# Kernel tuning notes

Measured on AMD Instinct MI355X. Metric: run time of the kernel, lower is better.

The kernel has to match this reference:

```python
import jax, jax.numpy as jnp
import numpy as np

B, IMG, TXT, DIM, H, D = 1, 1024, 256, 1536, 24, 64
SCALE = 1.0  # control cross-attn scale


def _lin(x, w, b):
    return x @ w + b


def _heads(x):  # [B,S,DIM] -> [B,H,S,D]
    return jnp.swapaxes(x.reshape(x.shape[0], x.shape[1], H, D), 1, 2)


def _merge(x):  # [B,H,S,D] -> [B,S,DIM]
    return jnp.swapaxes(x, 1, 2).reshape(x.shape[0], x.shape[2], H * D)


def _sdpa(q, k, v):
    s = jnp.einsum('bhqd,bhkd->bhqk', q, k) * (1.0 / np.sqrt(D))
    return jnp.einsum('bhqk,bhkd->bhqd', jax.nn.softmax(s, axis=-1), v)


def _rope(x, pe):  # x: [B,H,S,D], pe: [1,1,S,D//2,2,2]
    xr = x.reshape(*x.shape[:-1], -1, 1, 2)  # [B,H,S,D/2,1,2]
    out = pe[..., 0] * xr[..., 0] + pe[..., 1] * xr[..., 1]  # [B,H,S,D/2,2]
    return out.reshape(x.shape)


def _forward(hidden_states, encoder_hidden_states, hidden_states_control,
             encoder_hidden_states_control, img_to_q_control, pe,
             a_q_w, a_q_b, a_k_w, a_k_b, a_v_w, a_v_b,
             a_addq_w, a_addq_b, a_addk_w, a_addk_b, a_addv_w, a_addv_b,
             a_out_w, a_out_b, a_addout_w, a_addout_b,
             c_q_w, c_q_b, c_k_w, c_k_b, c_v_w, c_v_b,
             c_addq_w, c_addq_b, c_addk_w, c_addk_b, c_addv_w, c_addv_b,
             c_out_w, c_out_b, c_addout_w, c_addout_b):
    img_len = hidden_states.shape[1]
    # ---- main joint attention stream (no RoPE, per original) ----
    q = jnp.concatenate([_heads(_lin(hidden_states, a_q_w, a_q_b)),
                         _heads(_lin(encoder_hidden_states, a_addq_w, a_addq_b))], axis=2)
    k = jnp.concatenate([_heads(_lin(hidden_states, a_k_w, a_k_b)),
                         _heads(_lin(encoder_hidden_states, a_addk_w, a_addk_b))], axis=2)
    v = jnp.concatenate([_heads(_lin(hidden_states, a_v_w, a_v_b)),
                         _heads(_lin(encoder_hidden_states, a_addv_w, a_addv_b))], axis=2)
    hs = _merge(_sdpa(q, k, v))
    hs, ehs = hs[:, :img_len], hs[:, img_len:]
    # ---- control joint attention stream (with RoPE) ----
    qc = jnp.concatenate([_heads(_lin(hidden_states_control, c_q_w, c_q_b)),
                          _heads(_lin(encoder_hidden_states_control, c_addq_w, c_addq_b))], axis=2)
    kc = jnp.concatenate([_heads(_lin(hidden_states_control, c_k_w, c_k_b)),
                          _heads(_lin(encoder_hidden_states_control, c_addk_w, c_addk_b))], axis=2)
    vc = jnp.concatenate([_heads(_lin(hidden_states_control, c_v_w, c_v_b)),
                          _heads(_lin(encoder_hidden_states_control, c_addv_w, c_addv_b))], axis=2)
    key_cross, value_cross = kc, vc  # saved BEFORE RoPE, per original
    hsc = _merge(_sdpa(_rope(qc, pe), _rope(kc, pe), vc))
    hsc, ehsc = hsc[:, :img_len], hsc[:, img_len:]
    # ---- cross attention: img query attends to control K/V ----
    q_cross = _rope(_heads(img_to_q_control), pe[:, :, :img_len])
    k_cross = _rope(key_cross, pe[:, :, :key_cross.shape[2]])
    cross = _merge(_sdpa(q_cross, k_cross, value_cross))
    hs = hs + SCALE * cross
    # ---- output projections (to_out[1] is dropout p=0 -> identity) ----
    hs = _lin(hs, a_out_w, a_out_b)
    ehs = _lin(ehs, a_addout_w, a_addout_b)
    hsc = _lin(hsc, c_out_w, c_out_b)
    ehsc = _lin(ehsc, c_addout_w, c_addout_b)
    return hs, ehs, hsc, ehsc


def setup_inputs() -> dict:
    key = jax.random.key(0)
    ki = iter(jax.random.split(key, 80))
    d = {}
    d['hidden_states'] = jax.random.normal(next(ki), (B, IMG, DIM), jnp.float32)
    d['encoder_hidden_states'] = jax.random.normal(next(ki), (B, TXT, DIM), jnp.float32)
    d['hidden_states_control'] = jax.random.normal(next(ki), (B, IMG, DIM), jnp.float32)
    d['encoder_hidden_states_control'] = jax.random.normal(next(ki), (B, TXT, DIM), jnp.float32)
    d['img_to_q_control'] = jax.random.normal(next(ki), (B, IMG, DIM), jnp.float32)
    # realistic rotary pe: [1,1,S,D/2,2,2] rotation matrices
    S = IMG + TXT
    pos = np.arange(S, dtype=np.float32)
    freqs = 1.0 / (10000.0 ** (np.arange(0, D, 2, dtype=np.float32) / D))  # [D/2]
    ang = pos[:, None] * freqs[None, :]  # [S, D/2]
    cos, sin = np.cos(ang), np.sin(ang)
    pe = np.stack([np.stack([cos, -sin], -1), np.stack([sin, cos], -1)], -2)  # [S,D/2,2,2]
    d['pe'] = jnp.asarray(pe)[None, None]
    for p in ('a', 'c'):
        for name in ('q', 'k', 'v', 'addq', 'addk', 'addv', 'out', 'addout'):
            d[f'{p}_{name}_w'] = jax.random.normal(next(ki), (DIM, DIM), jnp.float32) * 0.02
            d[f'{p}_{name}_b'] = jax.random.normal(next(ki), (DIM,), jnp.float32) * 0.01
    return d


def reference(hidden_states, encoder_hidden_states, hidden_states_control,
              encoder_hidden_states_control, img_to_q_control, pe,
              a_q_w, a_q_b, a_k_w, a_k_b, a_v_w, a_v_b,
              a_addq_w, a_addq_b, a_addk_w, a_addk_b, a_addv_w, a_addv_b,
              a_out_w, a_out_b, a_addout_w, a_addout_b,
              c_q_w, c_q_b, c_k_w, c_k_b, c_v_w, c_v_b,
              c_addq_w, c_addq_b, c_addk_w, c_addk_b, c_addv_w, c_addv_b,
              c_out_w, c_out_b, c_addout_w, c_addout_b):
    return _forward(hidden_states, encoder_hidden_states, hidden_states_control,
                    encoder_hidden_states_control, img_to_q_control, pe,
                    a_q_w, a_q_b, a_k_w, a_k_b, a_v_w, a_v_b,
                    a_addq_w, a_addq_b, a_addk_w, a_addk_b, a_addv_w, a_addv_b,
                    a_out_w, a_out_b, a_addout_w, a_addout_b,
                    c_q_w, c_q_b, c_k_w, c_k_b, c_v_w, c_v_b,
                    c_addq_w, c_addq_b, c_addk_w, c_addk_b, c_addv_w, c_addv_b,
                    c_out_w, c_out_b, c_addout_w, c_addout_b)
```

## Files before the change

### kernel.cpp

```cpp
#include <hip/hip_runtime.h>

#define DIM 1536
#define IMG 1024
#define TXT 256
#define SEQ 1280
#define NH 24
#define HD 64
#define SD ((size_t)SEQ * DIM)
#define IDSZ ((size_t)IMG * DIM)
#define WSZ ((size_t)DIM * DIM)

typedef __attribute__((ext_vector_type(8))) short short8;
typedef __attribute__((ext_vector_type(4))) float f32x4;

__device__ __forceinline__ float bf2f(ushort u) {
    union { unsigned int i; float f; } v; v.i = ((unsigned int)u) << 16; return v.f;
}
__device__ __forceinline__ ushort f2bf(float f) {
    union { unsigned int i; float f; } v; v.f = f;
    unsigned int u = v.i;
    u += 0x7fffu + ((u >> 16) & 1u);
    return (ushort)(u >> 16);
}

__global__ __launch_bounds__(256) void detect_dtype(const void* __restrict__ p,
                                                    int* __restrict__ flag)
{
    __shared__ int cnt;
    if (threadIdx.x == 0) cnt = 0;
    __syncthreads();
    const ushort* u = (const ushort*)p;
    int local = 0;
    for (int i = threadIdx.x; i < 2048; i += 256) {
        ushort v = u[2 * i];
        int e = (v >> 7) & 0xFF;
        if (e >= 0xC0) local++;
    }
    atomicAdd(&cnt, local);
    __syncthreads();
    if (threadIdx.x == 0) flag[0] = (cnt > 16) ? 1 : 0;
}

struct CvtP {
    const void* src[16];
    ushort* dst[16];
    int n8[16];
};

__global__ __launch_bounds__(256) void convert_bf16(CvtP p, const int* __restrict__ dflag)
{
    const int a = blockIdx.y;
    const int i = blockIdx.x * 256 + threadIdx.x;
    if (i >= p.n8[a]) return;
    const size_t off = (size_t)i * 8;
    uint4 o;
    if (dflag[0]) {
        const float* s = (const float*)p.src[a] + off;
        const float4 f0 = *(const float4*)s;
        const float4 f1 = *(const float4*)(s + 4);
        ushort t[8];
        t[0] = f2bf(f0.x); t[1] = f2bf(f0.y); t[2] = f2bf(f0.z); t[3] = f2bf(f0.w);
        t[4] = f2bf(f1.x); t[5] = f2bf(f1.y); t[6] = f2bf(f1.z); t[7] = f2bf(f1.w);
        o = *(uint4*)t;
    } else {
        o = *(const uint4*)((const ushort*)p.src[a] + off);
    }
    *(uint4*)(p.dst[a] + off) = o;
}

#define LSTR 40

struct QKV3P {
    const ushort* Xb;
    const ushort* Wb;
    const void* B[12];
    float* Y[6];
    ushort* Yh[6];
    ushort* Yl[6];
};

__global__ __launch_bounds__(256) void gemm_qkv_v4(QKV3P p, const int* __restrict__ dflag)
{
    __shared__ __align__(16) ushort As[2][128 * LSTR];
    __shared__ __align__(16) ushort Bs[2][64 * 64];
    const int dt = dflag[0];
    const int bx = blockIdx.x;
    const int wsel = bx / 12;
    const int n0 = (bx - wsel * 12) * 128;
    const int ys = blockIdx.y;
    const int str = (ys >= 10) ? 1 : 0;
    const int m0g = (ys - str * 10) * 128;
    const bool istxt = (m0g >= IMG);
    const int widx = str * 6 + wsel + (istxt ? 3 : 0);
    const ushort* X  = p.Xb + (size_t)str * SD;
    const ushort* Wp = p.Wb + (size_t)widx * WSZ;
    const void* Bp = p.B[widx];
    const int yidx = str * 3 + wsel;
    float*  Y  = p.Y[yidx];
    ushort* yh = p.Yh[yidx];
// ... 50 lines not shown
    loadA(0); loadB(0);
    storeA(0); storeB(0);
    __syncthreads();

    for (int k = 0; k < DIM / 32; ++k) {
        const int cur = k & 1;
        const bool hn = (k + 1) < DIM / 32;
        if (hn) { loadA((k + 1) * 32); loadB((k + 1) * 32); }

        short8 b[4];
#pragma unroll
        for (int j = 0; j < 4; ++j) {
            const int rrn = wn + j * 16 + l16;
            const int R = rrn & 63, half = rrn >> 6;
            const int gx = (((half << 2) + quad) ^ (R & 7) ^ (R >> 3)) & 7;
            b[j] = *(const short8*)&Bs[cur][R * 64 + gx * 8];
        }
#pragma unroll
        for (int i = 0; i < 4; ++i) {
            const int rr = wm + i * 16 + l16;
            const int ps = (quad >> 1) ^ ((rr >> 3) & 1);
            const int col = ps * 16 + (quad & 1) * 8;
            short8 a = *(const short8*)&As[cur][rr * LSTR + col];
#pragma unroll
            for (int j = 0; j < 4; ++j)
                acc[i][j] = __builtin_amdgcn_mfma_f32_16x16x32_bf16(a, b[j], acc[i][j], 0, 0, 0);
        }
        if (hn) { storeA(cur ^ 1); storeB(cur ^ 1); }
        __syncthreads();
    }

#pragma unroll
    for (int j = 0; j < 4; ++j) {
        const int col = n0 + wn + j * 16 + l16;
        const float bv = dt ? ((const float*)Bp)[col] : bf2f(((const ushort*)Bp)[col]);
#pragma unroll
        for (int i = 0; i < 4; ++i)
#pragma unroll
            for (int r = 0; r < 4; ++r) {
                const int row = m0g + wm + i * 16 + quad * 4 + r;
                const size_t o = (size_t)row * DIM + col;
                const float val = acc[i][j][r] + bv;
                if (Y) Y[o] = val;
                if (yh) {
                    const ushort hv = f2bf(val);
                    yh[o] = hv;
                    yl[o] = f2bf(val - bf2f(hv));
                }
            }
    }
}

struct OutP {
    const float* X;
    const void* W[4]; const void* B[4];
    void* out;
};

__global__ __launch_bounds__(256) void gemm_out_v3(OutP p, const int* __restrict__ dflag)
{
    __shared__ __align__(16) ushort Ah[2][64 * LSTR];
    __shared__ __align__(16) ushort Al[2][64 * LSTR];
    __shared__ __align__(16) ushort Bs[2][64 * 64];
    const int dt = dflag[0];
    const int n0 = blockIdx.x * 128;
    const int mt = blockIdx.y;
    const int seg = (mt < 16) ? 0 : (mt < 20) ? 1 : (mt < 36) ? 2 : 3;
    const void* Wp = p.W[seg];
    const void* Bp = p.B[seg];
    const int m0 = mt * 64;

    const int t = threadIdx.x;
    const int wave = t >> 6, lane = t & 63;
    const int quad = lane >> 4, l16 = lane & 15;
    const int wm = (wave >> 1) * 32, wn = (wave & 1) * 64;

    const int arow = t >> 2, ag = t & 3;
    const int apg = ag >> 1, asub = ag & 1;
    const int aps = apg ^ ((arow >> 3) & 1);
    const int adst = arow * LSTR + aps * 16 + asub * 8;
    const int bn8 = (t & 15) << 3, bkk = (t >> 4) << 1;
    const int bkg = bkk >> 3, bo = bkk & 7;

    f32x4 acc[2][4];
#pragma unroll
    for (int i = 0; i < 2; ++i)
#pragma unroll
        for (int j = 0; j < 4; ++j) acc[i][j] = (f32x4)(0.0f);

    float4 raf[2];
    float4 rbf[4]; uint4 rbu[2];

    auto loadA = [&](int k0) {
        const float* xp = p.X + (size_t)(m0 + arow) * DIM + k0 + ag * 8;
        raf[0] = *(const float4*)xp;
        raf[1] = *(const float4*)(xp + 4);
    };
    auto loadB = [&](int k0) {
        const size_t off = (size_t)(k0 + bkk) * DIM + n0 + bn8;
        if (dt) {
            const float* wp0 = (const float*)Wp + off;
            rbf[0] = *(const float4*)wp0;         rbf[1] = *(const float4*)(wp0 + 4);
            rbf[2] = *(const float4*)(wp0 + DIM); rbf[3] = *(const float4*)(wp0 + DIM + 4);
        } else {
            const ushort* wp0 = (const ushort*)Wp + off;
            rbu[0] = *(const uint4*)wp0;
            rbu[1] = *(const uint4*)(wp0 + DIM);
        }
    };
    auto storeA = [&](int buf) {
        ushort hi[8], lo[8];
        const float* xs = (const float*)raf;
#pragma unroll
        for (int i = 0; i < 8; ++i) {
            hi[i] = f2bf(xs[i]);
            lo[i] = f2bf(xs[i] - bf2f(hi[i]));
        }
        *(uint4*)&Ah[buf][adst] = *(uint4*)&hi[0];
        *(uint4*)&Al[buf][adst] = *(uint4*)&lo[0];
    };
    auto storeB = [&](int buf) {
        ushort t0[8], t1[8];
        if (dt) {
            const float* f = (const float*)rbf;
#pragma unroll
            for (int j = 0; j < 8; ++j) { t0[j] = f2bf(f[j]); t1[j] = f2bf(f[8 + j]); }
        } else {
            *(uint4*)t0 = rbu[0];
            *(uint4*)t1 = rbu[1];
        }
#pragma unroll
        for (int j = 0; j < 8; ++j) {
            const int rr = bn8 + j;
            const int R = rr & 63, half = rr >> 6;
            const int gx = (((half << 2) + bkg) ^ (R & 7) ^ (R >> 3)) & 7;
            *(unsigned int*)&Bs[buf][R * 64 + gx * 8 + bo] =
                (unsigned int)t0[j] | ((unsigned int)t1[j] << 16);
        }
    };

    loadA(0); loadB(0);
    storeA(0); storeB(0);
    __syncthreads();

    for (int k = 0; k < DIM / 32; ++k) {
        const int cur = k & 1;
        const bool hn = (k + 1) < DIM / 32;
        if (hn) { loadA((k + 1) * 32); loadB((k + 1) * 32); }

        short8 b[4];
#pragma unroll
        for (int j = 0; j < 4; ++j) {
            const int rrn = wn + j * 16 + l16;
            const int R = rrn & 63, half = rrn >> 6;
            const int gx = (((half << 2) + quad) ^ (R & 7) ^ (R >> 3)) & 7;
            b[j] = *(const short8*)&Bs[cur][R * 64 + gx * 8];
        }
#pragma unroll
        for (int i = 0; i < 2; ++i) {
            const int rr = wm + i * 16 + l16;
            const int ps = (quad >> 1) ^ ((rr >> 3) & 1);
            const int col = ps * 16 + (quad & 1) * 8;
            short8 ah = *(const short8*)&Ah[cur][rr * LSTR + col];
            short8 al = *(const short8*)&Al[cur][rr * LSTR + col];
#pragma unroll
            for (int j = 0; j < 4; ++j) {
                acc[i][j] = __builtin_amdgcn_mfma_f32_16x16x32_bf16(ah, b[j], acc[i][j], 0, 0, 0);
                acc[i][j] = __builtin_amdgcn_mfma_f32_16x16x32_bf16(al, b[j], acc[i][j], 0, 0, 0);
            }
        }
        if (hn) { storeA(cur ^ 1); storeB(cur ^ 1); }
        __syncthreads();
    }

#pragma unroll
    for (int j = 0; j < 4; ++j) {
        const int col = n0 + wn + j * 16 + l16;
        const float bv = dt ? ((const float*)Bp)[col] : bf2f(((const ushort*)Bp)[col]);
#pragma unroll
        for (int i = 0; i < 2; ++i)
#pragma unroll
            for (int r = 0; r < 4; ++r) {
                const int grow = m0 + wm + i * 16 + quad * 4 + r;
                const size_t o = (size_t)grow * DIM + col;
                const float val = acc[i][j][r] + bv;
                if (dt) ((float*)p.out)[o] = val;
                else    ((ushort*)p.out)[o] = f2bf(val);
            }
    }
}

__device__ __forceinline__ void pe_load(const void* pe, int dt, size_t off,
                                        float& c00, float& c01, float& c10, float& c11)
{
    if (dt) {
        float4 pv = *(const float4*)((const float*)pe + off);
        c00 = pv.x; c01 = pv.y; c10 = pv.z; c11 = pv.w;
    } else {
        const ushort* pp = (const ushort*)pe + off;
        c00 = bf2f(pp[0]); c01 = bf2f(pp[1]); c10 = bf2f(pp[2]); c11 = bf2f(pp[3]);
    }
}

__global__ __launch_bounds__(256) void rope_f32_inplace(
    float* __restrict__ buf, const void* __restrict__ pe,
    const int* __restrict__ dflag, int S)
{
    const int dt = dflag[0];
    int idx = blockIdx.x * 256 + threadIdx.x;
    if (idx >= S * 768) return;
    int s = idx / 768, pp = idx - s * 768;
    int col = pp << 1, i = pp & 31;
    float* bp = buf + (size_t)s * DIM + col;
    float x0 = bp[0], x1 = bp[1];
    float c00, c01, c10, c11;
    pe_load(pe, dt, (size_t)s * 128 + i * 4, c00, c01, c10, c11);
    bp[0] = c00 * x0 + c01 * x1;
    bp[1] = c10 * x0 + c11 * x1;
}

__global__ __launch_bounds__(256) void rope_f32_to_split(
    const float* __restrict__ src, const void* __restrict__ pe,
    ushort* __restrict__ dh, ushort* __restrict__ dl,
    const int* __restrict__ dflag, int S)
{
    const int dt = dflag[0];
    int idx = blockIdx.x * 256 + threadIdx.x;
    if (idx >= S * 768) return;
    int s = idx / 768, pp = idx - s * 768;
    int col = pp << 1, i = pp & 31;
    float2 xv = *(const float2*)(src + (size_t)s * DIM + col);
    float c00, c01, c10, c11;
    pe_load(pe, dt, (size_t)s * 128 + i * 4, c00, c01, c10, c11);
    float y0 = c00 * xv.x + c01 * xv.y;
    float y1 = c10 * xv.x + c11 * xv.y;
    ushort h0 = f2bf(y0), h1 = f2bf(y1);
    ushort l0 = f2bf(y0 - bf2f(h0)), l1 = f2bf(y1 - bf2f(h1));
    *(unsigned int*)(dh + (size_t)s * DIM + col) = (unsigned int)h0 | ((unsigned int)h1 << 16);
    *(unsigned int*)(dl + (size_t)s * DIM + col) = (unsigned int)l0 | ((unsigned int)l1 << 16);
}

__global__ __launch_bounds__(256) void rope_in_to_f32(
    const void* __restrict__ src, const void* __restrict__ pe,
    float* __restrict__ dst, const int* __restrict__ dflag, int S)
{
    const int dt = dflag[0];
    int idx = blockIdx.x * 256 + threadIdx.x;
    if (idx >= S * 768) return;
    int s = idx / 768, pp = idx - s * 768;
    int col = pp << 1, i = pp & 31;
    float x0, x1;
    if (dt) {
        float2 xv = *(const float2*)((const float*)src + (size_t)s * DIM + col);
        x0 = xv.x; x1 = xv.y;
    } else {
        const ushort* sp = (const ushort*)src + (size_t)s * DIM + col;
        x0 = bf2f(sp[0]); x1 = bf2f(sp[1]);
    }
    float c00, c01, c10, c11;
    pe_load(pe, dt, (size_t)s * 128 + i * 4, c00, c01, c10, c11);
    float* dp = dst + (size_t)s * DIM + col;
    dp[0] = c00 * x0 + c01 * x1;
    dp[1] = c10 * x0 + c11 * x1;
}

__global__ __launch_bounds__(256) void vtrans_split(
    const float* __restrict__ V, ushort* __restrict__ Vth, ushort* __restrict__ Vtl,
    int seq)
{
    __shared__ unsigned int tile[64 * 65];
    const int s0 = blockIdx.x * 64;
    const int h = blockIdx.y;
    const int t = threadIdx.x;
#pragma unroll
    for (int it = 0; it < 16; ++it) {
        const int sl = (t >> 6) + (it << 2);
        const int d = t & 63;
        const float v = V[(size_t)(s0 + sl) * DIM + h * HD + d];
        const ushort hv = f2bf(v);
        const ushort lv = f2bf(v - bf2f(hv));
        tile[d * 65 + sl] = (unsigned int)hv | ((unsigned int)lv << 16);
    }
    __syncthreads();
    const int d = t >> 2, cc = (t & 3) << 4;
    ushort th[16], tl[16];
#pragma unroll
    for (int j = 0; j < 16; ++j) {
        const unsigned int w = tile[d * 65 + cc + j];
        th[j] = (ushort)w;
        tl[j] = (ushort)(w >> 16);
    }
    const size_t off = (size_t)(h * HD + d) * seq + s0 + cc;
    *(uint4*)(Vth + off)     = *(uint4*)&th[0];
    *(uint4*)(Vth + off + 8) = *(uint4*)&th[8];
    *(uint4*)(Vtl + off)     = *(uint4*)&tl[0];
    *(uint4*)(Vtl + off + 8) = *(uint4*)&tl[8];
}

__device__ __forceinline__ int swz(int row, int col) {
    return row * 64 + ((((col >> 3) ^ row) & 7) << 3) + (col & 7);
}
__device__ __forceinline__ short8 ldfrag(const ushort* plane, int row, int col) {
    return *(const short8*)&plane[swz(row, col)];
}

struct AttnP {
    const float* Qf;
    const ushort *Kh, *Kl, *Vth, *Vtl;
    float* Op0;
    float* Op1;
    float2* Ml;
    int kvchunk;
    int kvstride;
};

__global__ __launch_bounds__(256) void attn_mfma_split(AttnP p)
{
    __shared__ ushort Qh_[4096], Ql_[4096];
    __shared__ ushort Kh_[4096], Kl_[4096];
    __shared__ ushort Vh_[4096], Vl_[4096];

    const int q0 = blockIdx.x * 64;
    const int h = blockIdx.y;
    const int z = blockIdx.z;
    const int t = threadIdx.x;
    const int wave = t >> 6, lane = t & 63;
    const int quad = lane >> 4, l16 = lane & 15;
    const int wq0 = wave * 16;

    const int srow = t >> 2, c0 = (t & 3) << 4;
    const int g0 = c0 >> 3;
    const int p0 = ((g0 ^ (srow & 7)) & 7) << 3;
    const int p1 = (((g0 + 1) ^ (srow & 7)) & 7) << 3;

    {
        const float* src = p.Qf + (size_t)(q0 + srow) * DIM + h * HD + c0;
        float x[16];
        *(float4*)&x[0]  = *(const float4*)(src);
        *(float4*)&x[4]  = *(const float4*)(src + 4);
        *(float4*)&x[8]  = *(const float4*)(src + 8);
        *(float4*)&x[12] = *(const float4*)(src + 12);
        ushort hi[16], lo[16];
#pragma unroll
        for (int i = 0; i < 16; ++i) {
            hi[i] = f2bf(x[i]);
            lo[i] = f2bf(x[i] - bf2f(hi[i]));
        }
        *(uint4*)&Qh_[srow * 64 + p0] = *(uint4*)&hi[0];
        *(uint4*)&Qh_[srow * 64 + p1] = *(uint4*)&hi[8];
        *(uint4*)&Ql_[srow * 64 + p0] = *(uint4*)&lo[0];
        *(uint4*)&Ql_[srow * 64 + p1] = *(uint4*)&lo[8];
    }
    short8 qfh[2], qfl[2];
#pragma unroll
    for (int c = 0; c < 2; ++c) {
        qfh[c] = ldfrag(Qh_, wq0 + l16, c * 32 + quad * 8);
        qfl[c] = ldfrag(Ql_, wq0 + l16, c * 32 + quad * 8);
    }

    float m_[4], l_[4];
#pragma unroll
    for (int r = 0; r < 4; ++r) { m_[r] = -3e38f; l_[r] = 0.0f; }
    f32x4 Oacc[4];
#pragma unroll
    for (int j = 0; j < 4; ++j) Oacc[j] = (f32x4)(0.0f);

    const int kvbeg = z * p.kvchunk;
    for (int kt = 0; kt < p.kvchunk; kt += 64) {
        const int kv0 = kvbeg + kt;
        __syncthreads();
        {
            const size_t off = (size_t)(kv0 + srow) * DIM + h * HD + c0;
            *(uint4*)&Kh_[srow * 64 + p0] = *(const uint4*)(p.Kh + off);
            *(uint4*)&Kh_[srow * 64 + p1] = *(const uint4*)(p.Kh + off + 8);
            *(uint4*)&Kl_[srow * 64 + p0] = *(const uint4*)(p.Kl + off);
            *(uint4*)&Kl_[srow * 64 + p1] = *(const uint4*)(p.Kl + off + 8);
        }
        {
            const size_t off = (size_t)(h * HD + srow) * p.kvstride + kv0 + c0;
            *(uint4*)&Vh_[srow * 64 + p0] = *(const uint4*)(p.Vth + off);
            *(uint4*)&Vh_[srow * 64 + p1] = *(const uint4*)(p.Vth + off + 8);
            *(uint4*)&Vl_[srow * 64 + p0] = *(const uint4*)(p.Vtl + off);
            *(uint4*)&Vl_[srow * 64 + p1] = *(const uint4*)(p.Vtl + off + 8);
        }
        __syncthreads();

        f32x4 S[4];
#pragma unroll
        for (int j = 0; j < 4; ++j) S[j] = (f32x4)(0.0f);
#pragma unroll
        for (int c = 0; c < 2; ++c) {
#pragma unroll
            for (int j = 0; j < 4; ++j) {
                short8 bh = ldfrag(Kh_, j * 16 + l16, c * 32 + quad * 8);
                short8 bl = ldfrag(Kl_, j * 16 + l16, c * 32 + quad * 8);
                S[j] = __builtin_amdgcn_mfma_f32_16x16x32_bf16(qfh[c], bh, S[j], 0, 0, 0);
                S[j] = __builtin_amdgcn_mfma_f32_16x16x32_bf16(qfl[c], bh, S[j], 0, 0, 0);
                S[j] = __builtin_amdgcn_mfma_f32_16x16x32_bf16(qfh[c], bl, S[j], 0, 0, 0);
            }
        }
#pragma unroll
        for (int j = 0; j < 4; ++j)
#pragma unroll
            for (int r = 0; r < 4; ++r) S[j][r] *= 0.125f;

        float alpha[4];
#pragma unroll
        for (int r = 0; r < 4; ++r) {
            float mx = fmaxf(fmaxf(S[0][r], S[1][r]), fmaxf(S[2][r], S[3][r]));
            mx = fmaxf(mx, __shfl_xor(mx, 1));
            mx = fmaxf(mx, __shfl_xor(mx, 2));
            mx = fmaxf(mx, __shfl_xor(mx, 4));
            mx = fmaxf(mx, __shfl_xor(mx, 8));
            float mn = fmaxf(m_[r], mx);
            alpha[r] = __expf(m_[r] - mn);
            m_[r] = mn;
            float rs = 0.0f;
#pragma unroll
            for (int j = 0; j < 4; ++j) {
                float pv = __expf(S[j][r] - mn);
                S[j][r] = pv;
                rs += pv;
            }
            rs += __shfl_xor(rs, 1);
            rs += __shfl_xor(rs, 2);
            rs += __shfl_xor(rs, 4);
            rs += __shfl_xor(rs, 8);
            l_[r] = l_[r] * alpha[r] + rs;
        }
#pragma unroll
        for (int j = 0; j < 4; ++j)
#pragma unroll
            for (int r = 0; r < 4; ++r) Oacc[j][r] *= alpha[r];

        {
            const int prow = wq0 + quad * 4;
#pragma unroll
            for (int j = 0; j < 4; ++j)
#pragma unroll
                for (int r = 0; r < 4; ++r) {
                    float pv = S[j][r];
                    ushort ph = f2bf(pv);
                    ushort pl = f2bf(pv - bf2f(ph));
                    int idx = swz(prow + r, j * 16 + l16);
                    Qh_[idx] = ph;
                    Ql_[idx] = pl;
                }
        }

#pragma unroll
        for (int c = 0; c < 2; ++c) {
            short8 pah = ldfrag(Qh_, wq0 + l16, c * 32 + quad * 8);
            short8 pal = ldfrag(Ql_, wq0 + l16, c * 32 + quad * 8);
#pragma unroll
            for (int jn = 0; jn < 4; ++jn) {
                short8 vbh = ldfrag(Vh_, jn * 16 + l16, c * 32 + quad * 8);
                short8 vbl = ldfrag(Vl_, jn * 16 + l16, c * 32 + quad * 8);
                Oacc[jn] = __builtin_amdgcn_mfma_f32_16x16x32_bf16(pah, vbh, Oacc[jn], 0, 0, 0);
                Oacc[jn] = __builtin_amdgcn_mfma_f32_16x16x32_bf16(pal, vbh, Oacc[jn], 0, 0, 0);
                Oacc[jn] = __builtin_amdgcn_mfma_f32_16x16x32_bf16(pah, vbl, Oacc[jn], 0, 0, 0);
            }
        }
    }

    float* Opz = z ? p.Op1 : p.Op0;
#pragma unroll
    for (int r = 0; r < 4; ++r) {
        const int rowq = q0 + wq0 + quad * 4 + r;
        if (l16 == 0)
            p.Ml[((size_t)z * NH + h) * SEQ + rowq] = make_float2(m_[r], l_[r]);
#pragma unroll
        for (int jn = 0; jn < 4; ++jn)
            Opz[(size_t)rowq * DIM + h * HD + jn * 16 + l16] = Oacc[jn][r];
    }
}

__global__ __launch_bounds__(256) void attn_merge(
    const float* __restrict__ Op0, const float* __restrict__ Op1,
    const float2* __restrict__ Ml,
    float* __restrict__ out, const float* __restrict__ addto, int qlen)
{
    const int idx = blockIdx.x * 256 + threadIdx.x;
    if (idx >= qlen * 384) return;
    const int rowq = idx / 384;
    const int c4 = (idx - rowq * 384) << 2;
    const float2 a = Ml[(size_t)(c4 >> 6) * SEQ + rowq];
    const float2 b = Ml[(size_t)(NH + (c4 >> 6)) * SEQ + rowq];
    const float ms = fmaxf(a.x, b.x);
    const float s0 = __expf(a.x - ms), s1 = __expf(b.x - ms);
    const float inv = 1.0f / (s0 * a.y + s1 * b.y);
    const float4 o0 = *(const float4*)&Op0[(size_t)rowq * DIM + c4];
    const float4 o1 = *(const float4*)&Op1[(size_t)rowq * DIM + c4];
    float4 r;
    r.x = (s0 * o0.x + s1 * o1.x) * inv;
    r.y = (s0 * o0.y + s1 * o1.y) * inv;
    r.z = (s0 * o0.z + s1 * o1.z) * inv;
    r.w = (s0 * o0.w + s1 * o1.w) * inv;
    if (addto) {
        const float4 c = *(const float4*)&addto[(size_t)rowq * DIM + c4];
        r.x += c.x; r.y += c.y; r.z += c.z; r.w += c.w;
    }
    *(float4*)&out[(size_t)rowq * DIM + c4] = r;
}

extern "C" void kernel_launch(void* const* d_in, const int* in_sizes, int n_in,
                              void* d_out, int out_size, void* d_ws, size_t ws_size,
                              hipStream_t stream) {
    (void)in_sizes; (void)n_in; (void)out_size; (void)ws_size;
    const void* hs   = d_in[0];
    const void* ehs  = d_in[1];
    const void* hsc  = d_in[2];
    const void* ehsc = d_in[3];
    const void* i2q  = d_in[4];
    const void* pe   = d_in[5];
#define W_(i) ((const void*)d_in[i])

    int*   flag = (int*)d_ws;
    float* fb = (float*)((char*)d_ws + 256);
    float* q1 = fb;
    float* k1 = q1 + SD;
    float* v1 = k1 + SD;
    float* vC = v1 + SD;
    float* oA = vC + SD;
    float* oC = oA + SD;
    ushort* kh  = (ushort*)(oC + SD);
    ushort* klo = kh + SD;
    ushort* vth = klo + SD;
    ushort* vtl = vth + SD;
    ushort* Wbf = vtl + SD;
    ushort* Xbf = Wbf + 12 * WSZ;
    float2* Ml = (float2*)(Xbf + 2 * SD);
    float* qA = oC;
    float* qx = k1;

    dim3 blk(256);
    detect_dtype<<<1, blk, 0, stream>>>(hs, flag);

    {
        CvtP cp;
        const int wsrc[12] = {6, 8, 10, 12, 14, 16, 22, 24, 26, 28, 30, 32};
        for (int j = 0; j < 12; ++j) {
            cp.src[j] = W_(wsrc[j]);
            cp.dst[j] = Wbf + (size_t)j * WSZ;
            cp.n8[j] = (int)(WSZ / 8);
        }
        cp.src[12] = hs;   cp.dst[12] = Xbf;                cp.n8[12] = (int)(IDSZ / 8);
        cp.src[13] = ehs;  cp.dst[13] = Xbf + IDSZ;         cp.n8[13] = (int)((size_t)TXT * DIM / 8);
        cp.src[14] = hsc;  cp.dst[14] = Xbf + SD;           cp.n8[14] = (int)(IDSZ / 8);
        cp.src[15] = ehsc; cp.dst[15] = Xbf + SD + IDSZ;    cp.n8[15] = (int)((size_t)TXT * DIM / 8);
        convert_bf16<<<dim3((int)(WSZ / 8 + 255) / 256, 16), blk, 0, stream>>>(cp, flag);
    }

    QKV3P qp;
    qp.Xb = Xbf;
    qp.Wb = Wbf;
    {
        const int bsrc[12] = {7, 9, 11, 13, 15, 17, 23, 25, 27, 29, 31, 33};
        for (int j = 0; j < 12; ++j) qp.B[j] = W_(bsrc[j]);
    }
    for (int j = 0; j < 6; ++j) { qp.Y[j] = nullptr; qp.Yh[j] = nullptr; qp.Yl[j] = nullptr; }
    qp.Y[0] = qA;
    qp.Yh[1] = kh;  qp.Yl[1] = klo;
    qp.Y[2] = v1;
    qp.Y[3] = q1;
    qp.Y[4] = k1;
    qp.Y[5] = vC;
    gemm_qkv_v4<<<dim3(36, 20), blk, 0, stream>>>(qp, flag);

    auto ATTN = [&](const float* Qfp, int qblocks, float* Op0, float* Op1) {
        AttnP p;
        p.Qf = Qfp;
        p.Kh = kh;  p.Kl = klo;
        p.Vth = vth; p.Vtl = vtl;
        p.Op0 = Op0; p.Op1 = Op1; p.Ml = Ml;
        p.kvchunk = SEQ / 2; p.kvstride = SEQ;
        attn_mfma_split<<<dim3(qblocks, NH, 2), blk, 0, stream>>>(p);
    };

    vtrans_split<<<dim3(SEQ / 64, NH), blk, 0, stream>>>(v1, vth, vtl, SEQ);
    ATTN(qA, SEQ / 64, v1, oA);
    attn_merge<<<(SEQ * 384 + 255) / 256, blk, 0, stream>>>(v1, oA, Ml, oA, nullptr, SEQ);

    rope_f32_inplace<<<(SEQ * 768 + 255) / 256, blk, 0, stream>>>(q1, pe, flag, SEQ);
    rope_f32_to_split<<<(SEQ * 768 + 255) / 256, blk, 0, stream>>>(k1, pe, kh, klo, flag, SEQ);
    vtrans_split<<<dim3(SEQ / 64, NH), blk, 0, stream>>>(vC, vth, vtl, SEQ);
    rope_in_to_f32<<<(IMG * 768 + 255) / 256, blk, 0, stream>>>(i2q, pe, qx, flag, IMG);

    ATTN(q1, SEQ / 64, v1, vC);
    attn_merge<<<(SEQ * 384 + 255) / 256, blk, 0, stream>>>(v1, vC, Ml, oC, nullptr, SEQ);

    ATTN(qx, IMG / 64, v1, vC);
    attn_merge<<<(IMG * 384 + 255) / 256, blk, 0, stream>>>(v1, vC, Ml, oA, oA, IMG);

    OutP op;
    op.X = oA;
    op.W[0] = W_(18); op.B[0] = W_(19);
    op.W[1] = W_(20); op.B[1] = W_(21);
    op.W[2] = W_(34); op.B[2] = W_(35);
    op.W[3] = W_(36); op.B[3] = W_(37);
    op.out = d_out;
    gemm_out_v3<<<dim3(12, 40), blk, 0, stream>>>(op, flag);
#undef W_
}
```

Measured before the change: 654.9 us.

## Batch all attention passes into one launch and fuse prep and merge kernels

Merges the three separate attention launches into a single attn_all grid that indexes per-segment Q/K/V pointers. Each stream now gets its own K/V buffers, so the passes no longer serialize through shared scratch. The vtrans and three RoPE kernels are folded into one prep_fused launch, and the three attn_merge launches become one merge_all that writes bf16 hi/lo split activations directly. The output projection weights are pre-converted to bf16 in the convert pass, so gemm_out no longer converts per tile. The change also adds s_setprio around the MFMA loops, at the cost of more workspace memory and an extra weight conversion.

```diff
diff --git a/kernel.cpp b/kernel.cpp
--- a/kernel.cpp
+++ b/kernel.cpp
@@ -42,9 +42,9 @@
 }
 
 struct CvtP {
-    const void* src[16];
-    ushort* dst[16];
-    int n8[16];
+    const void* src[20];
+    ushort* dst[20];
+    int n8[20];
 };
 
 __global__ __launch_bounds__(256) void convert_bf16(CvtP p, const int* __restrict__ dflag)
@@ -201,12 +201,13 @@
 }
 
 struct OutP {
-    const float* X;
-    const void* W[4]; const void* B[4];
+    const ushort* Xh; const ushort* Xl;
+    const ushort* Wb;
+    const void* B[4];
     void* out;
 };
 
-__global__ __launch_bounds__(256) void gemm_out_v3(OutP p, const int* __restrict__ dflag)
+__global__ __launch_bounds__(256) void gemm_out_v4(OutP p, const int* __restrict__ dflag)
 {
     __shared__ __align__(16) ushort Ah[2][64 * LSTR];
     __shared__ __align__(16) ushort Al[2][64 * LSTR];
@@ -215,7 +216,7 @@
     const int n0 = blockIdx.x * 128;
     const int mt = blockIdx.y;
     const int seg = (mt < 16) ? 0 : (mt < 20) ? 1 : (mt < 36) ? 2 : 3;
-    const void* Wp = p.W[seg];
+    const ushort* Wp = p.Wb + (size_t)seg * WSZ;
     const void* Bp = p.B[seg];
     const int m0 = mt * 64;
 
@@ -237,47 +238,27 @@
 #pragma unroll
         for (int j = 0; j < 4; ++j) acc[i][j] = (f32x4)(0.0f);
 
-    float4 raf[2];
-    float4 rbf[4]; uint4 rbu[2];
+    uint4 rah, ral;
+    uint4 rbu[2];
 
     auto loadA = [&](int k0) {
-        const float* xp = p.X + (size_t)(m0 + arow) * DIM + k0 + ag * 8;
-        raf[0] = *(const float4*)xp;
-        raf[1] = *(const float4*)(xp + 4);
+        const size_t off = (size_t)(m0 + arow) * DIM + k0 + ag * 8;
+        rah = *(const uint4*)(p.Xh + off);
+        ral = *(const uint4*)(p.Xl + off);
     };
     auto loadB = [&](int k0) {
-        const size_t off = (size_t)(k0 + bkk) * DIM + n0 + bn8;
-        if (dt) {
-            const float* wp0 = (const float*)Wp + off;
-            rbf[0] = *(const float4*)wp0;         rbf[1] = *(const float4*)(wp0 + 4);
-            rbf[2] = *(const float4*)(wp0 + DIM); rbf[3] = *(const float4*)(wp0 + DIM + 4);
-        } else {
-            const ushort* wp0 = (const ushort*)Wp + off;
-            rbu[0] = *(const uint4*)wp0;
-            rbu[1] = *(const uint4*)(wp0 + DIM);
-        }
+        const ushort* wp0 = Wp + (size_t)(k0 + bkk) * DIM + n0 + bn8;
+        rbu[0] = *(const uint4*)wp0;
+        rbu[1] = *(const uint4*)(wp0 + DIM);
     };
     auto storeA = [&](int buf) {
-        ushort hi[8], lo[8];
-        const float* xs = (const float*)raf;
-#pragma unroll
-        for (int i = 0; i < 8; ++i) {
-            hi[i] = f2bf(xs[i]);
-            lo[i] = f2bf(xs[i] - bf2f(hi[i]));
-        }
-        *(uint4*)&Ah[buf][adst] = *(uint4*)&hi[0];
-        *(uint4*)&Al[buf][adst] = *(uint4*)&lo[0];
+        *(uint4*)&Ah[buf][adst] = rah;
+        *(uint4*)&Al[buf][adst] = ral;
     };
     auto storeB = [&](int buf) {
         ushort t0[8], t1[8];
-        if (dt) {
-            const float* f = (const float*)rbf;
-#pragma unroll
-            for (int j = 0; j < 8; ++j) { t0[j] = f2bf(f[j]); t1[j] = f2bf(f[8 + j]); }
-        } else {
-            *(uint4*)t0 = rbu[0];
-            *(uint4*)t1 = rbu[1];
-        }
+        *(uint4*)t0 = rbu[0];
+        *(uint4*)t1 = rbu[1];
 #pragma unroll
         for (int j = 0; j < 8; ++j) {
             const int rr = bn8 + j;
@@ -351,99 +332,104 @@
     }
 }
 
-__global__ __launch_bounds__(256) void rope_f32_inplace(
-    float* __restrict__ buf, const void* __restrict__ pe,
-    const int* __restrict__ dflag, int S)
-{
-    const int dt = dflag[0];
-    int idx = blockIdx.x * 256 + threadIdx.x;
-    if (idx >= S * 768) return;
-    int s = idx / 768, pp = idx - s * 768;
-    int col = pp << 1, i = pp & 31;
-    float* bp = buf + (size_t)s * DIM + col;
-    float x0 = bp[0], x1 = bp[1];
-    float c00, c01, c10, c11;
-    pe_load(pe, dt, (size_t)s * 128 + i * 4, c00, c01, c10, c11);
-    bp[0] = c00 * x0 + c01 * x1;
-    bp[1] = c10 * x0 + c11 * x1;
-}
-
-__global__ __launch_bounds__(256) void rope_f32_to_split(
-    const float* __restrict__ src, const void* __restrict__ pe,
-    ushort* __restrict__ dh, ushort* __restrict__ dl,
-    const int* __restrict__ dflag, int S)
-{
-    const int dt = dflag[0];
-    int idx = blockIdx.x * 256 + threadIdx.x;
-    if (idx >= S * 768) return;
-    int s = idx / 768, pp = idx - s * 768;
-    int col = pp << 1, i = pp & 31;
-    float2 xv = *(const float2*)(src + (size_t)s * DIM + col);
-    float c00, c01, c10, c11;
-    pe_load(pe, dt, (size_t)s * 128 + i * 4, c00, c01, c10, c11);
-    float y0 = c00 * xv.x + c01 * xv.y;
-    float y1 = c10 * xv.x + c11 * xv.y;
-    ushort h0 = f2bf(y0), h1 = f2bf(y1);
-    ushort l0 = f2bf(y0 - bf2f(h0)), l1 = f2bf(y1 - bf2f(h1));
-    *(unsigned int*)(dh + (size_t)s * DIM + col) = (unsigned int)h0 | ((unsigned int)h1 << 16);
-    *(unsigned int*)(dl + (size_t)s * DIM + col) = (unsigned int)l0 | ((unsigned int)l1 << 16);
-}
-
-__global__ __launch_bounds__(256) void rope_in_to_f32(
-    const void* __restrict__ src, const void* __restrict__ pe,
-    float* __restrict__ dst, const int* __restrict__ dflag, int S)
-{
-    const int dt = dflag[0];
-    int idx = blockIdx.x * 256 + threadIdx.x;
-    if (idx >= S * 768) return;
-    int s = idx / 768, pp = idx - s * 768;
-    int col = pp << 1, i = pp & 31;
-    float x0, x1;
-    if (dt) {
-        float2 xv = *(const float2*)((const float*)src + (size_t)s * DIM + col);
-        x0 = xv.x; x1 = xv.y;
-    } else {
-        const ushort* sp = (const ushort*)src + (size_t)s * DIM + col;
-        x0 = bf2f(sp[0]); x1 = bf2f(sp[1]);
-    }
-    float c00, c01, c10, c11;
-    pe_load(pe, dt, (size_t)s * 128 + i * 4, c00, c01, c10, c11);
-    float* dp = dst + (size_t)s * DIM + col;
-    dp[0] = c00 * x0 + c01 * x1;
-    dp[1] = c10 * x0 + c11 * x1;
-}
-
-__global__ __launch_bounds__(256) void vtrans_split(
-    const float* __restrict__ V, ushort* __restrict__ Vth, ushort* __restrict__ Vtl,
-    int seq)
+struct PrepP {
+    const float* v1; const float* vC;
+    ushort *vthA, *vtlA, *vthC, *vtlC;
+    float* q1;
+    const float* k1; ushort *khC, *kloC;
+    const void* i2q; float* qx;
+    const void* pe;
+};
+
+#define VT_BLKS 960
+#define RN0 (SEQ * 768)
+#define RN1 (SEQ * 768)
+#define RN2 (IMG * 768)
+
+__global__ __launch_bounds__(256) void prep_fused(PrepP p, const int* __restrict__ dflag)
 {
     __shared__ unsigned int tile[64 * 65];
-    const int s0 = blockIdx.x * 64;
-    const int h = blockIdx.y;
+    const int dt = dflag[0];
+    const int bx = blockIdx.x;
     const int t = threadIdx.x;
-#pragma unroll
-    for (int it = 0; it < 16; ++it) {
-        const int sl = (t >> 6) + (it << 2);
-        const int d = t & 63;
-        const float v = V[(size_t)(s0 + sl) * DIM + h * HD + d];
-        const ushort hv = f2bf(v);
-        const ushort lv = f2bf(v - bf2f(hv));
-        tile[d * 65 + sl] = (unsigned int)hv | ((unsigned int)lv << 16);
-    }
-    __syncthreads();
-    const int d = t >> 2, cc = (t & 3) << 4;
-    ushort th[16], tl[16];
-#pragma unroll
-    for (int j = 0; j < 16; ++j) {
-        const unsigned int w = tile[d * 65 + cc + j];
-        th[j] = (ushort)w;
-        tl[j] = (ushort)(w >> 16);
-    }
-    const size_t off = (size_t)(h * HD + d) * seq + s0 + cc;
-    *(uint4*)(Vth + off)     = *(uint4*)&th[0];
-    *(uint4*)(Vth + off + 8) = *(uint4*)&th[8];
-    *(uint4*)(Vtl + off)     = *(uint4*)&tl[0];
-    *(uint4*)(Vtl + off + 8) = *(uint4*)&tl[8];
+
+    if (bx < VT_BLKS) {
+        const int z = bx / 480, rem = bx - z * 480;
+        const int s0 = (rem % 20) * 64, h = rem / 20;
+        const float* V = z ? p.vC : p.v1;
+        ushort* Vth = z ? p.vthC : p.vthA;
+        ushort* Vtl = z ? p.vtlC : p.vtlA;
+#pragma unroll
+        for (int it = 0; it < 16; ++it) {
+            const int sl = (t >> 6) + (it << 2);
+            const int d = t & 63;
+            const float v = V[(size_t)(s0 + sl) * DIM + h * HD + d];
+            const ushort hv = f2bf(v);
+            const ushort lv = f2bf(v - bf2f(hv));
+            tile[d * 65 + sl] = (unsigned int)hv | ((unsigned int)lv << 16);
+        }
+        __syncthreads();
+        const int d = t >> 2, cc = (t & 3) << 4;
+        ushort th[16], tl[16];
+#pragma unroll
+        for (int j = 0; j < 16; ++j) {
+            const unsigned int w = tile[d * 65 + cc + j];
+            th[j] = (ushort)w;
+            tl[j] = (ushort)(w >> 16);
+        }
+        const size_t off = (size_t)(h * HD + d) * SEQ + s0 + cc;
+        *(uint4*)(Vth + off)     = *(uint4*)&th[0];
+        *(uint4*)(Vth + off + 8) = *(uint4*)&th[8];
+        *(uint4*)(Vtl + off)     = *(uint4*)&tl[0];
+        *(uint4*)(Vtl + off + 8) = *(uint4*)&tl[8];
+        return;
+    }
+
+    int idx = (bx - VT_BLKS) * 256 + t;
+    if (idx < RN0) {
+        int s = idx / 768, pp = idx - s * 768;
+        int col = pp << 1, i = pp & 31;
+        float* bp = p.q1 + (size_t)s * DIM + col;
+        float x0 = bp[0], x1 = bp[1];
+        float c00, c01, c10, c11;
+        pe_load(p.pe, dt, (size_t)s * 128 + i * 4, c00, c01, c10, c11);
+        bp[0] = c00 * x0 + c01 * x1;
+        bp[1] = c10 * x0 + c11 * x1;
+        return;
+    }
+    idx -= RN0;
+    if (idx < RN1) {
+        int s = idx / 768, pp = idx - s * 768;
+        int col = pp << 1, i = pp & 31;
+        float2 xv = *(const float2*)(p.k1 + (size_t)s * DIM + col);
+        float c00, c01, c10, c11;
+        pe_load(p.pe, dt, (size_t)s * 128 + i * 4, c00, c01, c10, c11);
+        float y0 = c00 * xv.x + c01 * xv.y;
+        float y1 = c10 * xv.x + c11 * xv.y;
+        ushort h0 = f2bf(y0), h1 = f2bf(y1);
+        ushort l0 = f2bf(y0 - bf2f(h0)), l1 = f2bf(y1 - bf2f(h1));
+        *(unsigned int*)(p.khC  + (size_t)s * DIM + col) = (unsigned int)h0 | ((unsigned int)h1 << 16);
+        *(unsigned int*)(p.kloC + (size_t)s * DIM + col) = (unsigned int)l0 | ((unsigned int)l1 << 16);
+        return;
+    }
+    idx -= RN1;
+    if (idx < RN2) {
+        int s = idx / 768, pp = idx - s * 768;
+        int col = pp << 1, i = pp & 31;
+        float x0, x1;
+        if (dt) {
+            float2 xv = *(const float2*)((const float*)p.i2q + (size_t)s * DIM + col);
+            x0 = xv.x; x1 = xv.y;
+        } else {
+            const ushort* sp = (const ushort*)p.i2q + (size_t)s * DIM + col;
+            x0 = bf2f(sp[0]); x1 = bf2f(sp[1]);
+        }
+        float c00, c01, c10, c11;
+        pe_load(p.pe, dt, (size_t)s * 128 + i * 4, c00, c01, c10, c11);
+        float* dp = p.qx + (size_t)s * DIM + col;
+        dp[0] = c00 * x0 + c01 * x1;
+        dp[1] = c10 * x0 + c11 * x1;
+    }
 }
 
 __device__ __forceinline__ int swz(int row, int col) {
@@ -453,23 +439,24 @@
     return *(const short8*)&plane[swz(row, col)];
 }
 
-struct AttnP {
-    const float* Qf;
-    const ushort *Kh, *Kl, *Vth, *Vtl;
-    float* Op0;
-    float* Op1;
-    float2* Ml;
-    int kvchunk;
-    int kvstride;
+struct AttnAllP {
+    const float* Qf[3];
+    const ushort* Kh[3]; const ushort* Kl[3];
+    const ushort* Vth[3]; const ushort* Vtl[3];
+    float* Op0[3]; float* Op1[3];
+    float2* Ml[3];
+    int mlq[3];
 };
 
-__global__ __launch_bounds__(256) void attn_mfma_split(AttnP p)
+__global__ __launch_bounds__(256) void attn_all(AttnAllP p)
 {
     __shared__ ushort Qh_[4096], Ql_[4096];
     __shared__ ushort Kh_[4096], Kl_[4096];
     __shared__ ushort Vh_[4096], Vl_[4096];
 
-    const int q0 = blockIdx.x * 64;
+    const int bx = blockIdx.x;
+    const int seg = (bx < 20) ? 0 : (bx < 40) ? 1 : 2;
+    const int q0 = (bx - ((seg == 0) ? 0 : (seg == 1) ? 20 : 40)) * 64;
     const int h = blockIdx.y;
     const int z = blockIdx.z;
     const int t = threadIdx.x;
@@ -477,13 +464,17 @@
     const int quad = lane >> 4, l16 = lane & 15;
     const int wq0 = wave * 16;
 
+    const float* Qf = p.Qf[seg];
+    const ushort* Kh = p.Kh[seg]; const ushort* Kl = p.Kl[seg];
+    const ushort* Vth = p.Vth[seg]; const ushort* Vtl = p.Vtl[seg];
+
     const int srow = t >> 2, c0 = (t & 3) << 4;
     const int g0 = c0 >> 3;
     const int p0 = ((g0 ^ (srow & 7)) & 7) << 3;
     const int p1 = (((g0 + 1) ^ (srow & 7)) & 7) << 3;
 
     {
-        const float* src = p.Qf + (size_t)(q0 + srow) * DIM + h * HD + c0;
+        const float* src = Qf + (size_t)(q0 + srow) * DIM + h * HD + c0;
         float x[16];
         *(float4*)&x[0]  = *(const float4*)(src);
         *(float4*)&x[4]  = *(const float4*)(src + 4);
@@ -514,29 +505,30 @@
 #pragma unroll
     for (int j = 0; j < 4; ++j) Oacc[j] = (f32x4)(0.0f);
 
-    const int kvbeg = z * p.kvchunk;
-    for (int kt = 0; kt < p.kvchunk; kt += 64) {
+    const int kvbeg = z * (SEQ / 2);
+    for (int kt = 0; kt < SEQ / 2; kt += 64) {
         const int kv0 = kvbeg + kt;
         __syncthreads();
         {
             const size_t off = (size_t)(kv0 + srow) * DIM + h * HD + c0;
-            *(uint4*)&Kh_[srow * 64 + p0] = *(const uint4*)(p.Kh + off);
-            *(uint4*)&Kh_[srow * 64 + p1] = *(const uint4*)(p.Kh + off + 8);
-            *(uint4*)&Kl_[srow * 64 + p0] = *(const uint4*)(p.Kl + off);
-            *(uint4*)&Kl_[srow * 64 + p1] = *(const uint4*)(p.Kl + off + 8);
+            *(uint4*)&Kh_[srow * 64 + p0] = *(const uint4*)(Kh + off);
+            *(uint4*)&Kh_[srow * 64 + p1] = *(const uint4*)(Kh + off + 8);
+            *(uint4*)&Kl_[srow * 64 + p0] = *(const uint4*)(Kl + off);
+            *(uint4*)&Kl_[srow * 64 + p1] = *(const uint4*)(Kl + off + 8);
         }
         {
-            const size_t off = (size_t)(h * HD + srow) * p.kvstride + kv0 + c0;
-            *(uint4*)&Vh_[srow * 64 + p0] = *(const uint4*)(p.Vth + off);
-            *(uint4*)&Vh_[srow * 64 + p1] = *(const uint4*)(p.Vth + off + 8);
-            *(uint4*)&Vl_[srow * 64 + p0] = *(const uint4*)(p.Vtl + off);
-            *(uint4*)&Vl_[srow * 64 + p1] = *(const uint4*)(p.Vtl + off + 8);
+            const size_t off = (size_t)(h * HD + srow) * SEQ + kv0 + c0;
+            *(uint4*)&Vh_[srow * 64 + p0] = *(const uint4*)(Vth + off);
+            *(uint4*)&Vh_[srow * 64 + p1] = *(const uint4*)(Vth + off + 8);
+            *(uint4*)&Vl_[srow * 64 + p0] = *(const uint4*)(Vtl + off);
+            *(uint4*)&Vl_[srow * 64 + p1] = *(const uint4*)(Vtl + off + 8);
         }
         __syncthreads();
 
         f32x4 S[4];
 #pragma unroll
         for (int j = 0; j < 4; ++j) S[j] = (f32x4)(0.0f);
+        __builtin_amdgcn_s_setprio(1);
 #pragma unroll
         for (int c = 0; c < 2; ++c) {
 #pragma unroll
@@ -548,6 +540,7 @@
                 S[j] = __builtin_amdgcn_mfma_f32_16x16x32_bf16(qfh[c], bl, S[j], 0, 0, 0);
             }
         }
+        __builtin_amdgcn_s_setprio(0);
 #pragma unroll
         for (int j = 0; j < 4; ++j)
 #pragma unroll
@@ -597,6 +590,7 @@
                 }
         }
 
+        __builtin_amdgcn_s_setprio(1);
 #pragma unroll
         for (int c = 0; c < 2; ++c) {
             short8 pah = ldfrag(Qh_, wq0 + l16, c * 32 + quad * 8);
@@ -610,46 +604,74 @@
                 Oacc[jn] = __builtin_amdgcn_mfma_f32_16x16x32_bf16(pah, vbl, Oacc[jn], 0, 0, 0);
             }
         }
-    }
-
-    float* Opz = z ? p.Op1 : p.Op0;
+        __builtin_amdgcn_s_setprio(0);
+    }
+
+    float* Opz = z ? p.Op1[seg] : p.Op0[seg];
+    const int mlq = p.mlq[seg];
+    float2* Ml = p.Ml[seg];
 #pragma unroll
     for (int r = 0; r < 4; ++r) {
         const int rowq = q0 + wq0 + quad * 4 + r;
         if (l16 == 0)
-            p.Ml[((size_t)z * NH + h) * SEQ + rowq] = make_float2(m_[r], l_[r]);
+            Ml[((size_t)z * NH + h) * mlq + rowq] = make_float2(m_[r], l_[r]);
 #pragma unroll
         for (int jn = 0; jn < 4; ++jn)
             Opz[(size_t)rowq * DIM + h * HD + jn * 16 + l16] = Oacc[jn][r];
     }
 }
 
-__global__ __launch_bounds__(256) void attn_merge(
-    const float* __restrict__ Op0, const float* __restrict__ Op1,
-    const float2* __restrict__ Ml,
-    float* __restrict__ out, const float* __restrict__ addto, int qlen)
+struct MergeP {
+    const float *pA0, *pA1, *pC0, *pC1, *pX0, *pX1;
+    const float2 *MlA, *MlC, *MlX;
+    ushort *Xh, *Xl;
+};
+
+__device__ __forceinline__ float4 comb2(const float* O0, const float* O1,
+                                        const float2* Ml, int mlq, int row, int c4)
 {
-    const int idx = blockIdx.x * 256 + threadIdx.x;
-    if (idx >= qlen * 384) return;
-    const int rowq = idx / 384;
-    const int c4 = (idx - rowq * 384) << 2;
-    const float2 a = Ml[(size_t)(c4 >> 6) * SEQ + rowq];
-    const float2 b = Ml[(size_t)(NH + (c4 >> 6)) * SEQ + rowq];
+    const int h = c4 >> 6;
+    const float2 a = Ml[(size_t)h * mlq + row];
+    const float2 b = Ml[(size_t)(NH + h) * mlq + row];
     const float ms = fmaxf(a.x, b.x);
     const float s0 = __expf(a.x - ms), s1 = __expf(b.x - ms);
     const float inv = 1.0f / (s0 * a.y + s1 * b.y);
-    const float4 o0 = *(const float4*)&Op0[(size_t)rowq * DIM + c4];
-    const float4 o1 = *(const float4*)&Op1[(size_t)rowq * DIM + c4];
+    const float4 o0 = *(const float4*)&O0[(size_t)row * DIM + c4];
+    const float4 o1 = *(const float4*)&O1[(size_t)row * DIM + c4];
     float4 r;
     r.x = (s0 * o0.x + s1 * o1.x) * inv;
     r.y = (s0 * o0.y + s1 * o1.y) * inv;
     r.z = (s0 * o0.z + s1 * o1.z) * inv;
     r.w = (s0 * o0.w + s1 * o1.w) * inv;
-    if (addto) {
-        const float4 c = *(const float4*)&addto[(size_t)rowq * DIM + c4];
-        r.x += c.x; r.y += c.y; r.z += c.z; r.w += c.w;
-    }
-    *(float4*)&out[(size_t)rowq * DIM + c4] = r;
+    return r;
+}
+
+__global__ __launch_bounds__(256) void merge_all(MergeP p)
+{
+    const int idx = blockIdx.x * 256 + threadIdx.x;
+    if (idx >= 2560 * 384) return;
+    const int row = idx / 384;
+    const int c4 = (idx - row * 384) << 2;
+    float4 r;
+    if (row < SEQ) {
+        r = comb2(p.pA0, p.pA1, p.MlA, SEQ, row, c4);
+        if (row < IMG) {
+            const float4 x = comb2(p.pX0, p.pX1, p.MlX, IMG, row, c4);
+            r.x += x.x; r.y += x.y; r.z += x.z; r.w += x.w;
+        }
+    } else {
+        r = comb2(p.pC0, p.pC1, p.MlC, SEQ, row - SEQ, c4);
+    }
+    float v[4] = {r.x, r.y, r.z, r.w};
+    ushort hi[4], lo[4];
+#pragma unroll
+    for (int j = 0; j < 4; ++j) {
+        hi[j] = f2bf(v[j]);
+        lo[j] = f2bf(v[j] - bf2f(hi[j]));
+    }
+    const size_t o = (size_t)row * DIM + c4;
+    *(uint2*)(p.Xh + o) = *(uint2*)hi;
+    *(uint2*)(p.Xl + o) = *(uint2*)lo;
 }
 
 extern "C" void kernel_launch(void* const* d_in, const int* in_sizes, int n_in,
@@ -664,40 +686,52 @@
     const void* pe   = d_in[5];
 #define W_(i) ((const void*)d_in[i])
 
-    int*   flag = (int*)d_ws;
-    float* fb = (float*)((char*)d_ws + 256);
-    float* q1 = fb;
-    float* k1 = q1 + SD;
-    float* v1 = k1 + SD;
-    float* vC = v1 + SD;
-    float* oA = vC + SD;
-    float* oC = oA + SD;
-    ushort* kh  = (ushort*)(oC + SD);
-    ushort* klo = kh + SD;
-    ushort* vth = klo + SD;
-    ushort* vtl = vth + SD;
-    ushort* Wbf = vtl + SD;
-    ushort* Xbf = Wbf + 12 * WSZ;
-    float2* Ml = (float2*)(Xbf + 2 * SD);
-    float* qA = oC;
-    float* qx = k1;
+    char* base = (char*)d_ws;
+    int* flag = (int*)base;
+    char* ptr = base + 256;
+    auto alloc = [&](size_t bytes) { char* r = ptr; ptr += bytes; return r; };
+    float* q1  = (float*)alloc(SD * 4);
+    float* k1  = (float*)alloc(SD * 4);
+    float* v1  = (float*)alloc(SD * 4);
+    float* vC  = (float*)alloc(SD * 4);
+    float* qA  = (float*)alloc(SD * 4);
+    float* qx  = (float*)alloc(IDSZ * 4);
+    ushort* khA  = (ushort*)alloc(SD * 2);
+    ushort* kloA = (ushort*)alloc(SD * 2);
+    ushort* vthA = (ushort*)alloc(SD * 2);
+    ushort* vtlA = (ushort*)alloc(SD * 2);
+    ushort* khC  = (ushort*)alloc(SD * 2);
+    ushort* kloC = (ushort*)alloc(SD * 2);
+    ushort* vthC = (ushort*)alloc(SD * 2);
+    ushort* vtlC = (ushort*)alloc(SD * 2);
+    float* pX0 = (float*)alloc(IDSZ * 4);
+    float* pX1 = (float*)alloc(IDSZ * 4);
+    float2* MlA = (float2*)alloc((size_t)2 * NH * SEQ * 8);
+    float2* MlC = (float2*)alloc((size_t)2 * NH * SEQ * 8);
+    float2* MlX = (float2*)alloc((size_t)2 * NH * IMG * 8);
+    ushort* Wbf = (ushort*)alloc(16 * WSZ * 2);
+    ushort* Xbf = (ushort*)alloc(2 * SD * 2);
+    float* pC1 = (float*)Xbf;
+    ushort* Xh = (ushort*)qA;
+    ushort* Xl = (ushort*)q1;
 
     dim3 blk(256);
     detect_dtype<<<1, blk, 0, stream>>>(hs, flag);
 
     {
         CvtP cp;
-        const int wsrc[12] = {6, 8, 10, 12, 14, 16, 22, 24, 26, 28, 30, 32};
-        for (int j = 0; j < 12; ++j) {
+        const int wsrc[16] = {6, 8, 10, 12, 14, 16, 22, 24, 26, 28, 30, 32,
+                              18, 20, 34, 36};
+        for (int j = 0; j < 16; ++j) {
             cp.src[j] = W_(wsrc[j]);
             cp.dst[j] = Wbf + (size_t)j * WSZ;
             cp.n8[j] = (int)(WSZ / 8);
         }
-        cp.src[12] = hs;   cp.dst[12] = Xbf;                cp.n8[12] = (int)(IDSZ / 8);
-        cp.src[13] = ehs;  cp.dst[13] = Xbf + IDSZ;         cp.n8[13] = (int)((size_t)TXT * DIM / 8);
-        cp.src[14] = hsc;  cp.dst[14] = Xbf + SD;           cp.n8[14] = (int)(IDSZ / 8);
-        cp.src[15] = ehsc; cp.dst[15] = Xbf + SD + IDSZ;    cp.n8[15] = (int)((size_t)TXT * DIM / 8);
-        convert_bf16<<<dim3((int)(WSZ / 8 + 255) / 256, 16), blk, 0, stream>>>(cp, flag);
+        cp.src[16] = hs;   cp.dst[16] = Xbf;             cp.n8[16] = (int)(IDSZ / 8);
+        cp.src[17] = ehs;  cp.dst[17] = Xbf + IDSZ;      cp.n8[17] = (int)((size_t)TXT * DIM / 8);
+        cp.src[18] = hsc;  cp.dst[18] = Xbf + SD;        cp.n8[18] = (int)(IDSZ / 8);
+        cp.src[19] = ehsc; cp.dst[19] = Xbf + SD + IDSZ; cp.n8[19] = (int)((size_t)TXT * DIM / 8);
+        convert_bf16<<<dim3((int)(WSZ / 8 + 255) / 256, 20), blk, 0, stream>>>(cp, flag);
     }
 
     QKV3P qp;
@@ -709,45 +743,59 @@
     }
     for (int j = 0; j < 6; ++j) { qp.Y[j] = nullptr; qp.Yh[j] = nullptr; qp.Yl[j] = nullptr; }
     qp.Y[0] = qA;
-    qp.Yh[1] = kh;  qp.Yl[1] = klo;
+    qp.Yh[1] = khA; qp.Yl[1] = kloA;
     qp.Y[2] = v1;
     qp.Y[3] = q1;
     qp.Y[4] = k1;
     qp.Y[5] = vC;
     gemm_qkv_v4<<<dim3(36, 20), blk, 0, stream>>>(qp, flag);
 
-    auto ATTN = [&](const float* Qfp, int qblocks, float* Op0, float* Op1) {
-        AttnP p;
-        p.Qf = Qfp;
-        p.Kh = kh;  p.Kl = klo;
-        p.Vth = vth; p.Vtl = vtl;
-        p.Op0 = Op0; p.Op1 = Op1; p.Ml = Ml;
-        p.kvchunk = SEQ / 2; p.kvstride = SEQ;
-        attn_mfma_split<<<dim3(qblocks, NH, 2), blk, 0, stream>>>(p);
-    };
-
-    vtrans_split<<<dim3(SEQ / 64, NH), blk, 0, stream>>>(v1, vth, vtl, SEQ);
-    ATTN(qA, SEQ / 64, v1, oA);
-    attn_merge<<<(SEQ * 384 + 255) / 256, blk, 0, stream>>>(v1, oA, Ml, oA, nullptr, SEQ);
-
-    rope_f32_inplace<<<(SEQ * 768 + 255) / 256, blk, 0, stream>>>(q1, pe, flag, SEQ);
-    rope_f32_to_split<<<(SEQ * 768 + 255) / 256, blk, 0, stream>>>(k1, pe, kh, klo, flag, SEQ);
-    vtrans_split<<<dim3(SEQ / 64, NH), blk, 0, stream>>>(vC, vth, vtl, SEQ);
-    rope_in_to_f32<<<(IMG * 768 + 255) / 256, blk, 0, stream>>>(i2q, pe, qx, flag, IMG);
-
-    ATTN(q1, SEQ / 64, v1, vC);
-    attn_merge<<<(SEQ * 384 + 255) / 256, blk, 0, stream>>>(v1, vC, Ml, oC, nullptr, SEQ);
-
-    ATTN(qx, IMG / 64, v1, vC);
-    attn_merge<<<(IMG * 384 + 255) / 256, blk, 0, stream>>>(v1, vC, Ml, oA, oA, IMG);
-
-    OutP op;
-    op.X = oA;
-    op.W[0] = W_(18); op.B[0] = W_(19);
-    op.W[1] = W_(20); op.B[1] = W_(21);
-    op.W[2] = W_(34); op.B[2] = W_(35);
-    op.W[3] = W_(36); op.B[3] = W_(37);
-    op.out = d_out;
-    gemm_out_v3<<<dim3(12, 40), blk, 0, stream>>>(op, flag);
+    {
+        PrepP pp;
+        pp.v1 = v1; pp.vC = vC;
+        pp.vthA = vthA; pp.vtlA = vtlA; pp.vthC = vthC; pp.vtlC = vtlC;
+        pp.q1 = q1;
+        pp.k1 = k1; pp.khC = khC; pp.kloC = kloC;
+        pp.i2q = i2q; pp.qx = qx;
+        pp.pe = pe;
+        const int ropeBlocks = (RN0 + RN1 + RN2 + 255) / 256;
+        prep_fused<<<VT_BLKS + ropeBlocks, blk, 0, stream>>>(pp, flag);
+    }
+
+    {
+        AttnAllP ap;
+        ap.Qf[0] = qA; ap.Qf[1] = q1; ap.Qf[2] = qx;
+        ap.Kh[0] = khA; ap.Kl[0] = kloA;
+        ap.Kh[1] = khC; ap.Kl[1] = kloC;
+        ap.Kh[2] = khC; ap.Kl[2] = kloC;
+        ap.Vth[0] = vthA; ap.Vtl[0] = vtlA;
+        ap.Vth[1] = vthC; ap.Vtl[1] = vtlC;
+        ap.Vth[2] = vthC; ap.Vtl[2] = vtlC;
+        ap.Op0[0] = v1;  ap.Op1[0] = k1;
+        ap.Op0[1] = vC;  ap.Op1[1] = pC1;
+        ap.Op0[2] = pX0; ap.Op1[2] = pX1;
+        ap.Ml[0] = MlA; ap.Ml[1] = MlC; ap.Ml[2] = MlX;
+        ap.mlq[0] = SEQ; ap.mlq[1] = SEQ; ap.mlq[2] = IMG;
+        attn_all<<<dim3(56, NH, 2), blk, 0, stream>>>(ap);
+    }
+
+    {
+        MergeP mp;
+        mp.pA0 = v1; mp.pA1 = k1;
+        mp.pC0 = vC; mp.pC1 = pC1;
+        mp.pX0 = pX0; mp.pX1 = pX1;
+        mp.MlA = MlA; mp.MlC = MlC; mp.MlX = MlX;
+        mp.Xh = Xh; mp.Xl = Xl;
+        merge_all<<<(2560 * 384 + 255) / 256, blk, 0, stream>>>(mp);
+    }
+
+    {
+        OutP op;
+        op.Xh = Xh; op.Xl = Xl;
+        op.Wb = Wbf + (size_t)12 * WSZ;
+        op.B[0] = W_(19); op.B[1] = W_(21); op.B[2] = W_(35); op.B[3] = W_(37);
+        op.out = d_out;
+        gemm_out_v4<<<dim3(12, 40), blk, 0, stream>>>(op, flag);
+    }
 #undef W_
 }
```

Measured after the change: 555.0 us. -15.3%, faster.
